# Kernel optimization log

Measured on AMD Instinct MI355X. Metric: run time of the kernel, lower is better.

Reference implementation:

```python
import jax, jax.numpy as jnp
import numpy as np
from jax import lax

H = 145; W = 145; BANDS = 200; D_MODEL = 128; NUM_CLASSES = 17
# Mamba2 defaults: expand=2, headdim=64, d_state=128, d_conv=4, ngroups=1
D_INNER = 256; NHEADS = 4; HEADDIM = 64; D_STATE = 128; D_CONV = 4
D_IN_PROJ = 2 * D_INNER + 2 * D_STATE + NHEADS  # 772
CONV_DIM = D_INNER + 2 * D_STATE                # 512


def _gelu(x):
    return jax.nn.gelu(x, approximate=False)


def _ln(x, g, b, eps=1e-5):
    m = jnp.mean(x, -1, keepdims=True)
    v = jnp.mean((x - m) ** 2, -1, keepdims=True)
    return (x - m) * lax.rsqrt(v + eps) * g + b


def _adaptive_pool_last(x, out):
    # PyTorch AdaptiveAvgPool semantics along the last axis via integral image
    L = x.shape[-1]
    i = np.arange(out)
    starts = (i * L) // out
    ends = -((-(i + 1) * L) // out)  # ceil((i+1)*L/out)
    cs = jnp.concatenate([jnp.zeros(x.shape[:-1] + (1,), x.dtype), jnp.cumsum(x, -1)], -1)
    return (cs[..., ends] - cs[..., starts]) / jnp.asarray(ends - starts, x.dtype)


def _mamba2(u, in_w, conv_w, conv_b, dt_bias, A_log, D, norm_w, out_w):
    # u: (L, D_MODEL). Faithful Mamba2 reference path (batch=1 squeezed).
    L = u.shape[0]
    zxbcdt = u @ in_w                      # (L, 772)
    z = zxbcdt[:, :D_INNER]                # (L, 256)
    xBC = zxbcdt[:, D_INNER:2 * D_INNER + 2 * D_STATE]  # (L, 512)
    dt = jax.nn.softplus(zxbcdt[:, -NHEADS:] + dt_bias)  # (L, 4)
    # causal depthwise conv1d, kernel D_CONV, then SiLU
    xp = jnp.pad(xBC, ((D_CONV - 1, 0), (0, 0)))
    xBC = sum(xp[k:k + L] * conv_w[:, k] for k in range(D_CONV)) + conv_b
    xBC = jax.nn.silu(xBC)
    xh = xBC[:, :D_INNER].reshape(L, NHEADS, HEADDIM)     # (L, h, p)
    Bm = xBC[:, D_INNER:D_INNER + D_STATE]                # (L, n)
    Cm = xBC[:, D_INNER + D_STATE:]                       # (L, n)
    A = -jnp.exp(A_log)                                   # (h,)

    def step(state, inp):
        dt_t, x_t, B_t, C_t = inp          # (h,), (h,p), (n,), (n,)
        dA = jnp.exp(dt_t * A)             # (h,)
        state = state * dA[:, None, None] + (dt_t[:, None] * x_t)[:, :, None] * B_t[None, None, :]
        y_t = jnp.einsum('hpn,n->hp', state, C_t)
        return state, y_t

    s0 = jnp.zeros((NHEADS, HEADDIM, D_STATE), u.dtype)
    _, y = lax.scan(step, s0, (dt, xh, Bm, Cm))           # y: (L, h, p)
    y = y + D[None, :, None] * xh
    y = y.reshape(L, D_INNER) * jax.nn.silu(z)            # gated
    y = y * lax.rsqrt(jnp.mean(y * y, -1, keepdims=True) + 1e-5) * norm_w  # RMSNormGated
    return y @ out_w                                      # (L, D_MODEL)


def _forward(x, ln_pre_g, ln_pre_b, fe_w1, fe_b1, fe_w2, fe_b2,
             cv_w1, cv_b1, cv_w2, cv_b2, mp_w, mp_b, mp_ln_g, mp_ln_b,
             m_in_w, m_conv_w, m_conv_b, m_dt_bias, m_A_log, m_D, m_norm_w, m_out_w,
             cls_ln_g, cls_ln_b, cls_w1, cls_b1, cls_w2, cls_b2, cls_w3, cls_b3):
    h, w, _ = x.shape
    xn = _ln(x, ln_pre_g, ln_pre_b)
    # MLP feature branch
    f = _gelu(xn @ fe_w1 + fe_b1)
    f = _gelu(f @ fe_w2 + fe_b2)                          # (h, w, 128)
    # conv branch
    c = jnp.transpose(xn, (2, 0, 1))[None]                # (1, bands, h, w)
    dn = ('NCHW', 'OIHW', 'NCHW')
    c = lax.conv_general_dilated(c, cv_w1, (1, 1), [(2, 2), (2, 2)], dimension_numbers=dn)
    c = _gelu(c + cv_b1[None, :, None, None])             # (1, 32, 147, 147)
    c = lax.conv_general_dilated(c, cv_w2, (1, 1), [(1, 1), (1, 1)], dimension_numbers=dn)
    c = _gelu(c + cv_b2[None, :, None, None])             # (1, 64, 147, 147)
    c = _adaptive_pool_last(c, W)                         # pool width -> 145
    c = _adaptive_pool_last(c.swapaxes(-1, -2), H).swapaxes(-1, -2)  # pool height
    conv_feat = jnp.transpose(c[0], (1, 2, 0))            # (145, 145, 64)
    comb = jnp.concatenate([f, conv_feat], -1).reshape(h * w, 192)
    p = _gelu(_ln(comb @ mp_w + mp_b, mp_ln_g, mp_ln_b))  # (L, d_model)
    m = _mamba2(p, m_in_w, m_conv_w, m_conv_b, m_dt_bias, m_A_log, m_D, m_norm_w, m_out_w)
    r = m.reshape(h, w, D_MODEL)
    o = _ln(r, cls_ln_g, cls_ln_b)
    o = _gelu(o @ cls_w1 + cls_b1)
    o = _gelu(o @ cls_w2 + cls_b2)
    return o @ cls_w3 + cls_b3                            # (h, w, num_classes)


def setup_inputs() -> dict:
    key = jax.random.key(0)
    ks = jax.random.split(key, 16)
    def n(k, shape, s=0.02):
        return jax.random.normal(k, shape, jnp.float32) * s
    return dict(
        x=jax.random.normal(ks[0], (H, W, BANDS), jnp.float32),
        ln_pre_g=jnp.ones((BANDS,), jnp.float32), ln_pre_b=jnp.zeros((BANDS,), jnp.float32),
        fe_w1=n(ks[1], (BANDS, 256)), fe_b1=jnp.zeros((256,), jnp.float32),
        fe_w2=n(ks[2], (256, 128)), fe_b2=jnp.zeros((128,), jnp.float32),
        cv_w1=n(ks[3], (32, BANDS, 3, 3)), cv_b1=jnp.zeros((32,), jnp.float32),
        cv_w2=n(ks[4], (64, 32, 3, 3)), cv_b2=jnp.zeros((64,), jnp.float32),
        mp_w=n(ks[5], (192, D_MODEL)), mp_b=jnp.zeros((D_MODEL,), jnp.float32),
        mp_ln_g=jnp.ones((D_MODEL,), jnp.float32), mp_ln_b=jnp.zeros((D_MODEL,), jnp.float32),
        m_in_w=n(ks[6], (D_MODEL, D_IN_PROJ)),
        m_conv_w=n(ks[7], (CONV_DIM, D_CONV), 0.2), m_conv_b=jnp.zeros((CONV_DIM,), jnp.float32),
        m_dt_bias=jnp.full((NHEADS,), -4.0, jnp.float32),
        m_A_log=jnp.log(jnp.linspace(1.0, 16.0, NHEADS)).astype(jnp.float32),
        m_D=jnp.ones((NHEADS,), jnp.float32),
        m_norm_w=jnp.ones((D_INNER,), jnp.float32),
        m_out_w=n(ks[8], (D_INNER, D_MODEL)),
        cls_ln_g=jnp.ones((D_MODEL,), jnp.float32), cls_ln_b=jnp.zeros((D_MODEL,), jnp.float32),
        cls_w1=n(ks[9], (D_MODEL, 128)), cls_b1=jnp.zeros((128,), jnp.float32),
        cls_w2=n(ks[10], (128, 64)), cls_b2=jnp.zeros((64,), jnp.float32),
        cls_w3=n(ks[11], (64, NUM_CLASSES)), cls_b3=jnp.zeros((NUM_CLASSES,), jnp.float32),
    )


def reference(x, ln_pre_g, ln_pre_b, fe_w1, fe_b1, fe_w2, fe_b2,
              cv_w1, cv_b1, cv_w2, cv_b2, mp_w, mp_b, mp_ln_g, mp_ln_b,
              m_in_w, m_conv_w, m_conv_b, m_dt_bias, m_A_log, m_D, m_norm_w, m_out_w,
              cls_ln_g, cls_ln_b, cls_w1, cls_b1, cls_w2, cls_b2, cls_w3, cls_b3):
    return _forward(x, ln_pre_g, ln_pre_b, fe_w1, fe_b1, fe_w2, fe_b2,
                    cv_w1, cv_b1, cv_w2, cv_b2, mp_w, mp_b, mp_ln_g, mp_ln_b,
                    m_in_w, m_conv_w, m_conv_b, m_dt_bias, m_A_log, m_D, m_norm_w, m_out_w,
                    cls_ln_g, cls_ln_b, cls_w1, cls_b1, cls_w2, cls_b2, cls_w3, cls_b3)
```

## Files before the change

### kernel.cpp

```cpp
#include <hip/hip_runtime.h>
#include <math.h>

#define HW 21025
#define Hdim 145
#define Wdim 145
#define NBANDS 200
#define CONVH 147
#define CONVHW 21609
#define QC 64
#define NCH 329
#define DTP 21056
#define SP 72
#define SSD_GRID 1344

typedef __attribute__((ext_vector_type(4))) float fv4;
typedef __attribute__((ext_vector_type(8))) short short8;

#define OFF_XN   ((size_t)0)
#define OFF_F1   ((size_t)4205000)
#define OFF_COMB ((size_t)9587400)
#define OFF_P    ((size_t)13624200)
#define OFF_ZX   ((size_t)16315400)
#define OFF_XBC  ((size_t)32546700)
#define OFF_S    ((size_t)43311500)
#define OFF_DT   ((size_t)54092172)
#define OFF_CT   ((size_t)54176396)
#define OFF_W    ((size_t)54177712)

__device__ __forceinline__ float gelu_f(float x){
    return 0.5f * x * (1.0f + erff(x * 0.70710678118654752440f));
}
__device__ __forceinline__ float silu_f(float x){
    return x / (1.0f + expf(-x));
}

__device__ __forceinline__ void bf16_split(float x, unsigned short& hs, unsigned short& ls){
    unsigned u = __float_as_uint(x);
    hs = (unsigned short)(u >> 16);
    float hif = __uint_as_float(u & 0xFFFF0000u);
    float lof = x - hif;
    ls = (unsigned short)(__float_as_uint(lof) >> 16);
}
__device__ __forceinline__ unsigned pack2(unsigned short a, unsigned short b){
    return (unsigned)a | ((unsigned)b << 16);
}
__device__ __forceinline__ unsigned packsplit(float x){
    unsigned short hs, ls;
    bf16_split(x, hs, ls);
    return ((unsigned)hs << 16) | (unsigned)ls;
}
__device__ __forceinline__ float unpackf(unsigned u){
    return __uint_as_float(u & 0xFFFF0000u) + __uint_as_float(u << 16);
}
__device__ __forceinline__ unsigned short bf16rnd(float x){
    unsigned u = __float_as_uint(x);
    unsigned r = u + 0x7FFFu + ((u >> 16) & 1u);
    return (unsigned short)(r >> 16);
}
__device__ __forceinline__ float bf16f(unsigned short h){
    return __uint_as_float((unsigned)h << 16);
}
__device__ __forceinline__ void unpack8(const unsigned* p, short8& h8, short8& l8){
    uint4 a = *reinterpret_cast<const uint4*>(p);
    uint4 b = *reinterpret_cast<const uint4*>(p + 4);
    unsigned v0 = a.x, v1 = a.y, v2 = a.z, v3 = a.w;
    unsigned v4 = b.x, v5 = b.y, v6 = b.z, v7 = b.w;
    h8[0]=(short)(v0>>16); l8[0]=(short)(v0&0xFFFFu);
    h8[1]=(short)(v1>>16); l8[1]=(short)(v1&0xFFFFu);
    h8[2]=(short)(v2>>16); l8[2]=(short)(v2&0xFFFFu);
    h8[3]=(short)(v3>>16); l8[3]=(short)(v3&0xFFFFu);
    h8[4]=(short)(v4>>16); l8[4]=(short)(v4&0xFFFFu);
    h8[5]=(short)(v5>>16); l8[5]=(short)(v5&0xFFFFu);
    h8[6]=(short)(v6>>16); l8[6]=(short)(v6&0xFFFFu);
    h8[7]=(short)(v7>>16); l8[7]=(short)(v7&0xFFFFu);
}

__device__ __forceinline__ bool gemm_decode(int bid, int NXB, int NYB, int& bx, int& by){
    int m = bid & 7;
    int r = bid >> 3;
    bx = r % NXB;
    by = (r / NXB) * 8 + m;
    return by < NYB;
}
__host__ __forceinline__ int gemm_grid(int NXB, int NYB){ return 8 * ((NYB + 7) / 8) * NXB; }

template<int ACT>
__global__ void ln_kernel(const float* __restrict__ in, const float* __restrict__ g,
                          const float* __restrict__ b, float* __restrict__ out, int D){
    int row = blockIdx.x, tid = threadIdx.x;
    const float* r = in + (size_t)row * D;
    float s = 0.f, s2 = 0.f;
    for (int i = tid; i < D; i += 256){ float v = r[i]; s += v; s2 += v*v; }
    __shared__ float r1[4], r2[4];
    #pragma unroll
    for (int o = 32; o > 0; o >>= 1){ s += __shfl_down(s, o); s2 += __shfl_down(s2, o); }
    if ((tid & 63) == 0){ r1[tid >> 6] = s; r2[tid >> 6] = s2; }
    __syncthreads();
    float S = r1[0] + r1[1] + r1[2] + r1[3];
    float S2 = r2[0] + r2[1] + r2[2] + r2[3];
    float mean = S / (float)D;
    float var = S2 / (float)D - mean * mean;
    float rs = rsqrtf(fmaxf(var, 0.f) + 1e-5f);
    float* o_ = out + (size_t)row * D;
    for (int i = tid; i < D; i += 256){
        float v = (r[i] - mean) * rs * g[i] + b[i];
        if (ACT == 1) v = gelu_f(v);
        o_[i] = v;
    }
}

template<int ACT, int MI, int ARMS>
__global__ __launch_bounds__(256) void gemm_mfma_w(const float* __restrict__ A, int lda,
                                                   const float* __restrict__ B, int ldb,
                                                   const float* __restrict__ bias,
                                                   const float* __restrict__ lng,
                                                   const float* __restrict__ lnb,
                                                   const float* __restrict__ arms_w,
                                                   float* __restrict__ C, int ldc,
                                                   int M, int N, int K, int NXB, int NYB){
    const int SA = 40;
    const int BM = MI * 32;
    __shared__ __align__(16) unsigned short Ah[BM * SA], Al[BM * SA];
    __shared__ __align__(16) unsigned short Bh[128 * SA], Bl[128 * SA];
    __shared__ float rs1[2][BM], rs2_[2][BM];
    __shared__ float ascale[BM];
    __shared__ float wn[256];
    int bx, by;
    if (!gemm_decode(blockIdx.x, NXB, NYB, bx, by)) return;
    int tid = threadIdx.x;
    int lane = tid & 63, wid = tid >> 6;
    int wy = wid >> 1, wx = wid & 1;
    int bm = by * BM, bn = bx * 128;
    int l15 = lane & 15, g = lane >> 4;

    if (ARMS){
        for (int i = tid; i < K && i < 256; i += 256) wn[i] = arms_w[i];
        int row = tid >> 2, seg = tid & 3;
        float ss = 0.f;
        if (row < BM && (bm + row) < M){
            const float* ar = A + (size_t)(bm + row) * lda + seg * (K >> 2);
            for (int k = 0; k < (K >> 2); k += 4){
                fv4 v = *reinterpret_cast<const fv4*>(ar + k);
                ss += v[0]*v[0] + v[1]*v[1] + v[2]*v[2] + v[3]*v[3];
            }
        }
        ss += __shfl_xor(ss, 1);
        ss += __shfl_xor(ss, 2);
        if ((tid & 3) == 0 && row < BM) ascale[row] = rsqrtf(ss / (float)K + 1e-5f);
        __syncthreads();
    }

    fv4 acc[MI][4];
    #pragma unroll
    for (int i = 0; i < MI; i++)
        #pragma unroll
        for (int j = 0; j < 4; j++) acc[i][j] = (fv4){0.f,0.f,0.f,0.f};

    int bcol = tid & 127;
    int bk16 = (tid >> 7) * 16;
    bool bcol_ok = (bn + bcol) < N;

    int nK = (K + 31) / 32;
    for (int ks = 0; ks < nK; ks++){
        int k0 = ks * 32;
        #pragma unroll
        for (int f = 0; f < MI; f++){
            int idx = tid * MI + f;
            int row = idx >> 3, qd = idx & 7;
            fv4 v = (fv4){0.f,0.f,0.f,0.f};
            if ((bm + row) < M && (k0 + qd * 4 + 4) <= K)
                v = *reinterpret_cast<const fv4*>(A + (size_t)(bm + row) * lda + k0 + qd * 4);
            if (ARMS) v *= ascale[row];
            unsigned short hs[4], ls[4];
            #pragma unroll
            for (int j = 0; j < 4; j++) bf16_split(v[j], hs[j], ls[j]);
            unsigned off = row * SA + qd * 4;
            *reinterpret_cast<uint2*>(&Ah[off]) = make_uint2(pack2(hs[0],hs[1]), pack2(hs[2],hs[3]));
            *reinterpret_cast<uint2*>(&Al[off]) = make_uint2(pack2(ls[0],ls[1]), pack2(ls[2],ls[3]));
        }
        {
            unsigned short hs[16], ls[16];
            #pragma unroll
            for (int j = 0; j < 16; j++){
                int kk = k0 + bk16 + j;
                float v = (bcol_ok && kk < K) ? B[(size_t)kk * ldb + bn + bcol] : 0.f;
                if (ARMS && kk < K) v *= wn[kk];
                bf16_split(v, hs[j], ls[j]);
            }
            unsigned off = bcol * SA + bk16;
            *reinterpret_cast<uint4*>(&Bh[off]) = make_uint4(pack2(hs[0],hs[1]), pack2(hs[2],hs[3]),
                                                             pack2(hs[4],hs[5]), pack2(hs[6],hs[7]));
            *reinterpret_cast<uint4*>(&Bh[off + 8]) = make_uint4(pack2(hs[8],hs[9]), pack2(hs[10],hs[11]),
                                                                 pack2(hs[12],hs[13]), pack2(hs[14],hs[15]));
            *reinterpret_cast<uint4*>(&Bl[off]) = make_uint4(pack2(ls[0],ls[1]), pack2(ls[2],ls[3]),
                                                             pack2(ls[4],ls[5]), pack2(ls[6],ls[7]));
            *reinterpret_cast<uint4*>(&Bl[off + 8]) = make_uint4(pack2(ls[8],ls[9]), pack2(ls[10],ls[11]),
                                                                 pack2(ls[12],ls[13]), pack2(ls[14],ls[15]));
        }
        __syncthreads();
        short8 afh[MI], afl[MI], bfh[4], bfl[4];
        #pragma unroll
        for (int mi = 0; mi < MI; mi++){
            unsigned off = (wy * (MI * 16) + mi * 16 + l15) * SA + g * 8;
            afh[mi] = *reinterpret_cast<const short8*>(&Ah[off]);
            afl[mi] = *reinterpret_cast<const short8*>(&Al[off]);
        }
        #pragma unroll
        for (int ni = 0; ni < 4; ni++){
            unsigned off = (wx * 64 + ni * 16 + l15) * SA + g * 8;
            bfh[ni] = *reinterpret_cast<const short8*>(&Bh[off]);
            bfl[ni] = *reinterpret_cast<const short8*>(&Bl[off]);
        }
        #pragma unroll
        for (int mi = 0; mi < MI; mi++)
            #pragma unroll
            for (int ni = 0; ni < 4; ni++){
                acc[mi][ni] = __builtin_amdgcn_mfma_f32_16x16x32_bf16(afh[mi], bfh[ni], acc[mi][ni], 0, 0, 0);
                acc[mi][ni] = __builtin_amdgcn_mfma_f32_16x16x32_bf16(afh[mi], bfl[ni], acc[mi][ni], 0, 0, 0);
                acc[mi][ni] = __builtin_amdgcn_mfma_f32_16x16x32_bf16(afl[mi], bfh[ni], acc[mi][ni], 0, 0, 0);
            }
        __syncthreads();
    }
    float bv[4], lgv[4], lbv[4];
    #pragma unroll
    for (int ni = 0; ni < 4; ni++){
        int cc = bn + wx * 64 + ni * 16 + l15;
        bool ok = cc < N;
        bv[ni]  = (bias && ok) ? bias[cc] : 0.f;
        if (ACT >= 2){ lgv[ni] = ok ? lng[cc] : 1.f; lbv[ni] = ok ? lnb[cc] : 0.f; }
    }
    if (ACT >= 2){
        #pragma unroll
        for (int mi = 0; mi < MI; mi++)
            #pragma unroll
            for (int j = 0; j < 4; j++){
                float s = 0.f, s2 = 0.f;
                #pragma unroll
                for (int ni = 0; ni < 4; ni++){
                    float v = acc[mi][ni][j] + bv[ni];
                    s += v; s2 += v * v;
                }
                #pragma unroll
                for (int o = 1; o < 16; o <<= 1){
                    s += __shfl_xor(s, o); s2 += __shfl_xor(s2, o);
                }
                int row = wy * (MI * 16) + mi * 16 + g * 4 + j;
                if (l15 == 0){ rs1[wx][row] = s; rs2_[wx][row] = s2; }
            }
        __syncthreads();
        #pragma unroll
        for (int mi = 0; mi < MI; mi++)
            #pragma unroll
            for (int j = 0; j < 4; j++){
                int row = wy * (MI * 16) + mi * 16 + g * 4 + j;
                int rr = bm + row;
                if (rr >= M) continue;
                float S = rs1[0][row] + rs1[1][row];
                float S2 = rs2_[0][row] + rs2_[1][row];
                float mean = S / 128.f;
                float var = S2 / 128.f - mean * mean;
                float rsq = rsqrtf(fmaxf(var, 0.f) + 1e-5f);
                #pragma unroll
                for (int ni = 0; ni < 4; ni++){
                    int cc = bn + wx * 64 + ni * 16 + l15;
                    float v = acc[mi][ni][j] + bv[ni];
                    v = (v - mean) * rsq * lgv[ni] + lbv[ni];
                    if (ACT == 3) v = gelu_f(v);
                    C[(size_t)rr * ldc + cc] = v;
                }
            }
    } else {
        #pragma unroll
        for (int mi = 0; mi < MI; mi++)
            #pragma unroll
            for (int ni = 0; ni < 4; ni++){
                int cc = bn + wx * 64 + ni * 16 + l15;
                if (cc >= N) continue;
                #pragma unroll
                for (int j = 0; j < 4; j++){
                    int rr = bm + wy * (MI * 16) + mi * 16 + g * 4 + j;
                    if (rr >= M) continue;
                    float v = acc[mi][ni][j] + bv[ni];
                    if (ACT == 1) v = gelu_f(v);
                    C[(size_t)rr * ldc + cc] = v;
                }
            }
    }
}

__global__ __launch_bounds__(256) void cls_tail(const float* __restrict__ A,
                                                const float* __restrict__ W2,
                                                const float* __restrict__ b2,
                                                const float* __restrict__ W3,
                                                const float* __restrict__ b3,
                                                float* __restrict__ out,
                                                int M, int NYB){
    const int SA = 40;
    __shared__ __align__(16) unsigned short Ah[64 * SA], Al[64 * SA];
    __shared__ __align__(16) unsigned short Bh[64 * SA], Bl[64 * SA];
    __shared__ __align__(16) unsigned short A2h[64 * 72], A2l[64 * 72];
    __shared__ __align__(16) unsigned short B3h[32 * 72], B3l[32 * 72];
    int bx, by;
    if (!gemm_decode(blockIdx.x, 1, NYB, bx, by)) return;
    int tid = threadIdx.x;
    int lane = tid & 63, wid = tid >> 6;
    int wy = wid >> 1, wx = wid & 1;
    int bm = by * 64;
    int l15 = lane & 15, g = lane >> 4;

    for (int e = tid; e < 2048; e += 256){
        int n = e >> 6, k = e & 63;
        float v = (n < 17) ? W3[(size_t)k * 17 + n] : 0.f;
        unsigned short hs, ls;
        bf16_split(v, hs, ls);
        B3h[n * 72 + k] = hs;
        B3l[n * 72 + k] = ls;
    }

    fv4 acc[2][2];
    #pragma unroll
    for (int mi = 0; mi < 2; mi++)
        #pragma unroll
        for (int ni = 0; ni < 2; ni++) acc[mi][ni] = (fv4){0.f,0.f,0.f,0.f};

    int bn_t = tid & 63;
    int bk8 = (tid >> 6) * 8;
    #pragma unroll
    for (int ks = 0; ks < 4; ks++){
        int k0 = ks * 32;
        #pragma unroll
        for (int f = 0; f < 2; f++){
            int idx = tid * 2 + f;
            int row = idx >> 3, qd = idx & 7;
            fv4 v = (fv4){0.f,0.f,0.f,0.f};
            if ((bm + row) < M)
                v = *reinterpret_cast<const fv4*>(A + (size_t)(bm + row) * 128 + k0 + qd * 4);
            unsigned short hs[4], ls[4];
            #pragma unroll
            for (int j = 0; j < 4; j++) bf16_split(v[j], hs[j], ls[j]);
            unsigned off = row * SA + qd * 4;
            *reinterpret_cast<uint2*>(&Ah[off]) = make_uint2(pack2(hs[0],hs[1]), pack2(hs[2],hs[3]));
            *reinterpret_cast<uint2*>(&Al[off]) = make_uint2(pack2(ls[0],ls[1]), pack2(ls[2],ls[3]));
        }
        {
            unsigned short hs[8], ls[8];
            #pragma unroll
            for (int j = 0; j < 8; j++){
                int kk = k0 + bk8 + j;
                float v = W2[(size_t)kk * 64 + bn_t];
                bf16_split(v, hs[j], ls[j]);
            }
            unsigned off = bn_t * SA + bk8;
            *reinterpret_cast<uint4*>(&Bh[off]) = make_uint4(pack2(hs[0],hs[1]), pack2(hs[2],hs[3]),
                                                             pack2(hs[4],hs[5]), pack2(hs[6],hs[7]));
            *reinterpret_cast<uint4*>(&Bl[off]) = make_uint4(pack2(ls[0],ls[1]), pack2(ls[2],ls[3]),
                                                             pack2(ls[4],ls[5]), pack2(ls[6],ls[7]));
        }
        __syncthreads();
        short8 afh[2], afl[2], bfh[2], bfl[2];
        #pragma unroll
        for (int mi = 0; mi < 2; mi++){
            unsigned off = (wy * 32 + mi * 16 + l15) * SA + g * 8;
            afh[mi] = *reinterpret_cast<const short8*>(&Ah[off]);
            afl[mi] = *reinterpret_cast<const short8*>(&Al[off]);
        }
        #pragma unroll
        for (int ni = 0; ni < 2; ni++){
            unsigned off = (wx * 32 + ni * 16 + l15) * SA + g * 8;
            bfh[ni] = *reinterpret_cast<const short8*>(&Bh[off]);
            bfl[ni] = *reinterpret_cast<const short8*>(&Bl[off]);
        }
        #pragma unroll
        for (int mi = 0; mi < 2; mi++)
            #pragma unroll
            for (int ni = 0; ni < 2; ni++){
                acc[mi][ni] = __builtin_amdgcn_mfma_f32_16x16x32_bf16(afh[mi], bfh[ni], acc[mi][ni], 0, 0, 0);
                acc[mi][ni] = __builtin_amdgcn_mfma_f32_16x16x32_bf16(afh[mi], bfl[ni], acc[mi][ni], 0, 0, 0);
                acc[mi][ni] = __builtin_amdgcn_mfma_f32_16x16x32_bf16(afl[mi], bfh[ni], acc[mi][ni], 0, 0, 0);
            }
        __syncthreads();
    }
    #pragma unroll
    for (int mi = 0; mi < 2; mi++)
        #pragma unroll
        for (int ni = 0; ni < 2; ni++){
            int col = wx * 32 + ni * 16 + l15;
            float bv = b2[col];
            #pragma unroll
            for (int j = 0; j < 4; j++){
                int row = wy * 32 + mi * 16 + g * 4 + j;
                float v = gelu_f(acc[mi][ni][j] + bv);
                unsigned short hs, ls;
                bf16_split(v, hs, ls);
                A2h[row * 72 + col] = hs;
                A2l[row * 72 + col] = ls;
            }
        }
    __syncthreads();
    fv4 acc3[2];
    acc3[0] = (fv4){0.f,0.f,0.f,0.f};
    acc3[1] = (fv4){0.f,0.f,0.f,0.f};
    #pragma unroll
    for (int ks = 0; ks < 2; ks++){
        unsigned aoff = (wid * 16 + l15) * 72 + ks * 32 + g * 8;
        short8 a2h = *reinterpret_cast<const short8*>(&A2h[aoff]);
        short8 a2l = *reinterpret_cast<const short8*>(&A2l[aoff]);
        #pragma unroll
        for (int ni = 0; ni < 2; ni++){
            unsigned boff = (ni * 16 + l15) * 72 + ks * 32 + g * 8;
            short8 b3h_ = *reinterpret_cast<const short8*>(&B3h[boff]);
            short8 b3l_ = *reinterpret_cast<const short8*>(&B3l[boff]);
            acc3[ni] = __builtin_amdgcn_mfma_f32_16x16x32_bf16(a2h, b3h_, acc3[ni], 0, 0, 0);
            acc3[ni] = __builtin_amdgcn_mfma_f32_16x16x32_bf16(a2h, b3l_, acc3[ni], 0, 0, 0);
            acc3[ni] = __builtin_amdgcn_mfma_f32_16x16x32_bf16(a2l, b3h_, acc3[ni], 0, 0, 0);
        }
    }
    #pragma unroll
    for (int ni = 0; ni < 2; ni++){
        int col = ni * 16 + l15;
        if (col >= 17) continue;
        float bv = b3[col];
        #pragma unroll
        for (int j = 0; j < 4; j++){
            int row = bm + wid * 16 + g * 4 + j;
            if (row >= M) continue;
            out[(size_t)row * 17 + col] = acc3[ni][j] + bv;
        }
    }
}

__global__ __launch_bounds__(256) void dt_from_p(const float* __restrict__ p,
                                                 const float* __restrict__ w,
                                                 const float* __restrict__ dtb,
                                                 float* __restrict__ dtbT){
    __shared__ float wl[512];
    int tid = threadIdx.x;
    for (int i = tid; i < 512; i += 256){
        int k = i >> 2, h = i & 3;
        wl[i] = w[(size_t)k * 772 + 768 + h];
// ... 268 lines not shown
__global__ __launch_bounds__(64) void ssd_phaseB(unsigned short* __restrict__ Sb,
                                                 const float* __restrict__ chunkT){
    __shared__ float e[NCH];
    int tid = threadIdx.x;
    int idx = blockIdx.x * 64 + tid;
    int h = idx >> 13, pn = idx & 8191;
    for (int c = tid; c < NCH; c += 64) e[c] = __expf(chunkT[c * 4 + h]);
    __syncthreads();
    #define ADDR_(cc) Sb[((size_t)((cc) * 4 + h)) * 8192 + pn]
    unsigned short r0 = ADDR_(0), r1 = ADDR_(1), r2 = ADDR_(2), r3 = ADDR_(3);
    float s = 0.f;
    int c = 0;
    for (; c + 8 <= NCH; c += 4){
        unsigned short n0 = ADDR_(c + 4), n1 = ADDR_(c + 5), n2 = ADDR_(c + 6), n3 = ADDR_(c + 7);
        ADDR_(c) = bf16rnd(s);     s = fmaf(s, e[c],     bf16f(r0));
        ADDR_(c + 1) = bf16rnd(s); s = fmaf(s, e[c + 1], bf16f(r1));
        ADDR_(c + 2) = bf16rnd(s); s = fmaf(s, e[c + 2], bf16f(r2));
        ADDR_(c + 3) = bf16rnd(s); s = fmaf(s, e[c + 3], bf16f(r3));
        r0 = n0; r1 = n1; r2 = n2; r3 = n3;
    }
    for (; c < NCH; c++){
        unsigned short nx = (c + 4 < NCH) ? ADDR_(c + 4) : (unsigned short)0;
        float loc = bf16f(r0); r0 = r1; r1 = r2; r2 = r3; r3 = nx;
        ADDR_(c) = bf16rnd(s);
        s = fmaf(s, e[c], loc);
    }
    #undef ADDR_
}

__global__ __launch_bounds__(256) void ssd_phaseC(const unsigned* __restrict__ xbcp,
                                                  const float* __restrict__ zx,
                                                  const float* __restrict__ dtbT,
                                                  const float* __restrict__ A_log,
                                                  const float* __restrict__ Dvec,
                                                  const unsigned short* __restrict__ Sb,
                                                  float* __restrict__ y){
    __shared__ __align__(16) unsigned short U0[64 * SP];
    __shared__ __align__(16) unsigned short U1h[64 * SP], U1l[64 * SP];
    __shared__ float cum[64], dth[64];
    int c, h;
    if (!ssd_decode(blockIdx.x, c, h)) return;
    int t0 = c * QC, Q = min(QC, HW - t0);
    int tid = threadIdx.x;
    chunk_cumsum_t(dtbT, t0, Q, h, A_log, cum, dth);
    int lane = tid & 63, wid = tid >> 6;
    int wy = wid >> 1, wx = wid & 1;
    int l15 = lane & 15, g = lane >> 4;

    int trow[2], srow[2], prow[2];
    #pragma unroll
    for (int i = 0; i < 2; i++){
        trow[i] = min(t0 + wy * 32 + i * 16 + l15, HW - 1);
        srow[i] = min(t0 + wx * 32 + i * 16 + l15, HW - 1);
        prow[i] = wx * 32 + i * 16 + l15;
    }

    fv4 accG[2][2], accA[2][2];
    #pragma unroll
    for (int mi = 0; mi < 2; mi++)
        #pragma unroll
        for (int ni = 0; ni < 2; ni++){ accG[mi][ni] = (fv4){0.f,0.f,0.f,0.f}; accA[mi][ni] = (fv4){0.f,0.f,0.f,0.f}; }

    const unsigned short* Sbase = Sb + (size_t)(c * 4 + h) * 8192;
    #pragma unroll
    for (int k0 = 0; k0 < 128; k0 += 32){
        short8 ah[2], al[2], bh[2], bl[2], sh[2];
        #pragma unroll
        for (int mi = 0; mi < 2; mi++)
            unpack8(xbcp + (size_t)trow[mi] * 512 + 384 + k0 + g * 8, ah[mi], al[mi]);
        #pragma unroll
        for (int ni = 0; ni < 2; ni++){
            unpack8(xbcp + (size_t)srow[ni] * 512 + 256 + k0 + g * 8, bh[ni], bl[ni]);
            sh[ni] = *reinterpret_cast<const short8*>(Sbase + prow[ni] * 128 + k0 + g * 8);
        }
        #pragma unroll
        for (int mi = 0; mi < 2; mi++)
            #pragma unroll
            for (int ni = 0; ni < 2; ni++){
                accG[mi][ni] = __builtin_amdgcn_mfma_f32_16x16x32_bf16(ah[mi], bh[ni], accG[mi][ni], 0, 0, 0);
                accG[mi][ni] = __builtin_amdgcn_mfma_f32_16x16x32_bf16(ah[mi], bl[ni], accG[mi][ni], 0, 0, 0);
                accG[mi][ni] = __builtin_amdgcn_mfma_f32_16x16x32_bf16(al[mi], bh[ni], accG[mi][ni], 0, 0, 0);
                accA[mi][ni] = __builtin_amdgcn_mfma_f32_16x16x32_bf16(ah[mi], sh[ni], accA[mi][ni], 0, 0, 0);
                accA[mi][ni] = __builtin_amdgcn_mfma_f32_16x16x32_bf16(al[mi], sh[ni], accA[mi][ni], 0, 0, 0);
            }
    }
    #pragma unroll
    for (int mi = 0; mi < 2; mi++)
        #pragma unroll
        for (int ni = 0; ni < 2; ni++)
            #pragma unroll
            for (int j = 0; j < 4; j++){
                int t = wy * 32 + mi * 16 + g * 4 + j;
                int s = wx * 32 + ni * 16 + l15;
                float pv = 0.f;
                if (s <= t && s < Q)
                    pv = accG[mi][ni][j] * __expf(cum[t] - cum[s]) * dth[s];
                U0[t * SP + s] = bf16rnd(pv);
            }
    for (int e2 = tid; e2 < 2048; e2 += 256){
        int pp = e2 & 63, sp = e2 >> 6;
        int s0 = 2 * sp;
        unsigned v0 = (s0 < Q)     ? xbcp[(size_t)(t0 + s0) * 512 + h * 64 + pp] : 0u;
        unsigned v1 = (s0 + 1 < Q) ? xbcp[(size_t)(t0 + s0 + 1) * 512 + h * 64 + pp] : 0u;
        *reinterpret_cast<unsigned*>(&U1h[pp * SP + s0]) = pack2((unsigned short)(v0 >> 16), (unsigned short)(v1 >> 16));
        *reinterpret_cast<unsigned*>(&U1l[pp * SP + s0]) = pack2((unsigned short)(v0 & 0xFFFFu), (unsigned short)(v1 & 0xFFFFu));
    }
    __syncthreads();
    fv4 accY[2][2];
    #pragma unroll
    for (int mi = 0; mi < 2; mi++)
        #pragma unroll
        for (int ni = 0; ni < 2; ni++)
            #pragma unroll
            for (int j = 0; j < 4; j++){
                int t = wy * 32 + mi * 16 + g * 4 + j;
                accY[mi][ni][j] = __expf(cum[t]) * accA[mi][ni][j];
            }
    #pragma unroll
    for (int kk = 0; kk < 2; kk++){
        short8 ph[2], xh[2], xl[2];
        #pragma unroll
        for (int mi = 0; mi < 2; mi++){
            unsigned off = (wy * 32 + mi * 16 + l15) * SP + kk * 32 + g * 8;
            ph[mi] = *reinterpret_cast<const short8*>(&U0[off]);
        }
        #pragma unroll
        for (int ni = 0; ni < 2; ni++){
            unsigned off = (wx * 32 + ni * 16 + l15) * SP + kk * 32 + g * 8;
            xh[ni] = *reinterpret_cast<const short8*>(&U1h[off]);
            xl[ni] = *reinterpret_cast<const short8*>(&U1l[off]);
        }
        #pragma unroll
        for (int mi = 0; mi < 2; mi++)
            #pragma unroll
            for (int ni = 0; ni < 2; ni++){
                accY[mi][ni] = __builtin_amdgcn_mfma_f32_16x16x32_bf16(ph[mi], xh[ni], accY[mi][ni], 0, 0, 0);
                accY[mi][ni] = __builtin_amdgcn_mfma_f32_16x16x32_bf16(ph[mi], xl[ni], accY[mi][ni], 0, 0, 0);
            }
    }
    float Dh = Dvec[h];
    #pragma unroll
    for (int mi = 0; mi < 2; mi++)
        #pragma unroll
        for (int ni = 0; ni < 2; ni++)
            #pragma unroll
            for (int j = 0; j < 4; j++){
                int t = wy * 32 + mi * 16 + g * 4 + j;
                if (t >= Q) continue;
                int p = wx * 32 + ni * 16 + l15;
                float xv = unpackf(xbcp[(size_t)(t0 + t) * 512 + h * 64 + p]);
                float zv = zx[(size_t)(t0 + t) * 772 + h * 64 + p];
                y[(size_t)(t0 + t) * 256 + h * 64 + p] = (accY[mi][ni][j] + Dh * xv) * silu_f(zv);
            }
}

extern "C" void kernel_launch(void* const* d_in, const int* in_sizes, int n_in,
                              void* d_out, int out_size, void* d_ws, size_t ws_size,
                              hipStream_t stream){
    (void)in_sizes; (void)n_in; (void)out_size; (void)ws_size;
    const float* x        = (const float*)d_in[0];
    const float* ln_pre_g = (const float*)d_in[1];
    const float* ln_pre_b = (const float*)d_in[2];
    const float* fe_w1    = (const float*)d_in[3];
    const float* fe_b1    = (const float*)d_in[4];
    const float* fe_w2    = (const float*)d_in[5];
    const float* fe_b2    = (const float*)d_in[6];
    const float* cv_w1    = (const float*)d_in[7];
    const float* cv_b1    = (const float*)d_in[8];
    const float* cv_w2    = (const float*)d_in[9];
    const float* cv_b2    = (const float*)d_in[10];
    const float* mp_w     = (const float*)d_in[11];
    const float* mp_b     = (const float*)d_in[12];
    const float* mp_ln_g  = (const float*)d_in[13];
    const float* mp_ln_b  = (const float*)d_in[14];
    const float* m_in_w   = (const float*)d_in[15];
    const float* m_conv_w = (const float*)d_in[16];
    const float* m_conv_b = (const float*)d_in[17];
    const float* m_dtb    = (const float*)d_in[18];
    const float* m_A_log  = (const float*)d_in[19];
    const float* m_D      = (const float*)d_in[20];
    const float* m_norm_w = (const float*)d_in[21];
    const float* m_out_w  = (const float*)d_in[22];
    const float* cls_ln_g = (const float*)d_in[23];
    const float* cls_ln_b = (const float*)d_in[24];
    const float* cls_w1   = (const float*)d_in[25];
    const float* cls_b1   = (const float*)d_in[26];
    const float* cls_w2   = (const float*)d_in[27];
    const float* cls_b2   = (const float*)d_in[28];
    const float* cls_w3   = (const float*)d_in[29];
    const float* cls_b3   = (const float*)d_in[30];

    float* ws   = (float*)d_ws;
    float* xn   = ws + OFF_XN;
    float* f1   = ws + OFF_F1;
    float* comb = ws + OFF_COMB;
    float* p    = ws + OFF_P;
    float* zx   = ws + OFF_ZX;
    unsigned* xbcp = (unsigned*)(ws + OFF_XBC);
    unsigned short* Sb = (unsigned short*)(ws + OFF_S);
    float* dtbT = ws + OFF_DT;
    float* chkT = ws + OFF_CT;
    float* c1h  = ws + OFF_XBC;
    float* c2h  = ws + OFF_XBC + 691488;
    float* ybuf = ws + OFF_F1;
    float* cls0 = ws + OFF_XN;
    float* cls1 = ws + OFF_P;
    unsigned short* W1h = (unsigned short*)(ws + OFF_W);
    unsigned short* W1l = (unsigned short*)(ws + OFF_W + 32256);
    unsigned short* W2h = (unsigned short*)(ws + OFF_W + 64512);
    unsigned short* W2l = (unsigned short*)(ws + OFF_W + 73728);
    const float* NUL = (const float*)nullptr;

    prep_w<200, 32, 7><<<(32 * 2016 + 255) / 256, 256, 0, stream>>>(cv_w1, W1h, W1l);
    prep_w<32, 64, 1><<<(64 * 288 + 255) / 256, 256, 0, stream>>>(cv_w2, W2h, W2l);
    ln_kernel<0><<<HW, 256, 0, stream>>>(x, ln_pre_g, ln_pre_b, xn, NBANDS);
    gemm_mfma_w<1, 4, 0><<<gemm_grid(2, 165), 256, 0, stream>>>(xn, 200, fe_w1, 256, fe_b1,
        NUL, NUL, NUL, f1, 256, HW, 256, 200, 2, 165);
    gemm_mfma_w<1, 2, 0><<<gemm_grid(1, 329), 256, 0, stream>>>(f1, 256, fe_w2, 128, fe_b2,
        NUL, NUL, NUL, comb, 192, HW, 128, 256, 1, 329);
    conv_mfma<200, 32, 2, 7, 1><<<dim3(3, CONVH), 256, 0, stream>>>(xn, Hdim, Wdim, W1h, W1l, cv_b1, c1h);
    conv_mfma<32, 64, 1, 1, 2><<<dim3(3, CONVH), 256, 0, stream>>>(c1h, CONVH, CONVH, W2h, W2l, cv_b2, c2h);
    pool_kernel<<<(HW * 64 + 255) / 256, 256, 0, stream>>>(c2h, comb);
    gemm_mfma_w<3, 2, 0><<<gemm_grid(1, 329), 256, 0, stream>>>(comb, 192, mp_w, 128, mp_b,
        mp_ln_g, mp_ln_b, NUL, p, 128, HW, 128, 192, 1, 329);
    gemm_mfma_w<0, 4, 0><<<gemm_grid(6, 165), 256, 0, stream>>>(p, 128, m_in_w, 772,
        NUL, NUL, NUL, NUL, zx, 772, HW, 768, 128, 6, 165);
    dt_from_p<<<(HW + 63) / 64, 256, 0, stream>>>(p, m_in_w, m_dtb, dtbT);
    conv1d_tiled<<<dim3(4, NCH), 256, 0, stream>>>(zx, m_conv_w, m_conv_b, xbcp);
    ssd_phaseA<<<SSD_GRID, 256, 0, stream>>>(xbcp, dtbT, m_A_log, Sb, chkT);
    ssd_phaseB<<<512, 64, 0, stream>>>(Sb, chkT);
    ssd_phaseC<<<SSD_GRID, 256, 0, stream>>>(xbcp, zx, dtbT, m_A_log, m_D, Sb, ybuf);
    gemm_mfma_w<2, 2, 1><<<gemm_grid(1, 329), 256, 0, stream>>>(ybuf, 256, m_out_w, 128,
        NUL, cls_ln_g, cls_ln_b, m_norm_w, cls0, 128, HW, 128, 256, 1, 329);
    gemm_mfma_w<1, 2, 0><<<gemm_grid(1, 329), 256, 0, stream>>>(cls0, 128, cls_w1, 128, cls_b1,
        NUL, NUL, NUL, cls1, 128, HW, 128, 128, 1, 329);
    cls_tail<<<gemm_grid(1, 329), 256, 0, stream>>>(cls1, cls_w2, cls_b2, cls_w3, cls_b3,
        (float*)d_out, HW, 329);
}
```

Baseline: 475.0 us.

## Replace LDS-staged GEMM with direct-load MFMA GEMM using pre-split packed weights

```diff
diff --git a/kernel.cpp b/kernel.cpp
--- a/kernel.cpp
+++ b/kernel.cpp
@@ -26,6 +26,15 @@
 #define OFF_DT   ((size_t)54092172)
 #define OFF_CT   ((size_t)54176396)
 #define OFF_W    ((size_t)54177712)
+#define OFF_WG   ((size_t)54260656)
+
+#define WG_FE1   0
+#define WG_FE2   57344
+#define WG_MP    90112
+#define WG_IN    114688
+#define WG_OUT   212992
+#define WG_CLS1  245760
+#define WG_TOTAL 262144
 
 __device__ __forceinline__ float gelu_f(float x){
     return 0.5f * x * (1.0f + erff(x * 0.70710678118654752440f));
@@ -74,6 +83,14 @@
     h8[6]=(short)(v6>>16); l8[6]=(short)(v6&0xFFFFu);
     h8[7]=(short)(v7>>16); l8[7]=(short)(v7&0xFFFFu);
 }
+__device__ __forceinline__ void split8f(fv4 a0, fv4 a1, short8& h8, short8& l8){
+    unsigned short hs, ls;
+    #pragma unroll
+    for (int j = 0; j < 4; j++){
+        bf16_split(a0[j], hs, ls); h8[j] = (short)hs; l8[j] = (short)ls;
+        bf16_split(a1[j], hs, ls); h8[4 + j] = (short)hs; l8[4 + j] = (short)ls;
+    }
+}
 
 __device__ __forceinline__ bool gemm_decode(int bid, int NXB, int NYB, int& bx, int& by){
     int m = bid & 7;
@@ -109,182 +126,126 @@
     }
 }
 
-template<int ACT, int MI, int ARMS>
-__global__ __launch_bounds__(256) void gemm_mfma_w(const float* __restrict__ A, int lda,
-                                                   const float* __restrict__ B, int ldb,
+__global__ void prep_fc(const float* __restrict__ fe_w1, const float* __restrict__ fe_w2,
+                        const float* __restrict__ mp_w, const float* __restrict__ in_w,
+                        const float* __restrict__ out_w, const float* __restrict__ cls_w1,
+                        unsigned* __restrict__ Wg){
+    int idx = blockIdx.x * 256 + threadIdx.x;
+    if (idx >= WG_TOTAL) return;
+    const float* src; int Ksrc, Kp, ld, local;
+    if (idx < WG_FE2)      { src = fe_w1;  Ksrc = 200; Kp = 224; ld = 256; local = idx; }
+    else if (idx < WG_MP)  { src = fe_w2;  Ksrc = 256; Kp = 256; ld = 128; local = idx - WG_FE2; }
+    else if (idx < WG_IN)  { src = mp_w;   Ksrc = 192; Kp = 192; ld = 128; local = idx - WG_MP; }
+    else if (idx < WG_OUT) { src = in_w;   Ksrc = 128; Kp = 128; ld = 772; local = idx - WG_IN; }
+    else if (idx < WG_CLS1){ src = out_w;  Ksrc = 256; Kp = 256; ld = 128; local = idx - WG_OUT; }
+    else                   { src = cls_w1; Ksrc = 128; Kp = 128; ld = 128; local = idx - WG_CLS1; }
+    int col = local / Kp, k = local % Kp;
+    float v = (k < Ksrc) ? src[(size_t)k * ld + col] : 0.f;
+    Wg[idx] = packsplit(v);
+}
+
+template<int ACT, int MF>
+__global__ __launch_bounds__(256) void gemm_direct(const float* __restrict__ A, int lda,
+                                                   const unsigned* __restrict__ Wg,
                                                    const float* __restrict__ bias,
                                                    const float* __restrict__ lng,
                                                    const float* __restrict__ lnb,
-                                                   const float* __restrict__ arms_w,
                                                    float* __restrict__ C, int ldc,
-                                                   int M, int N, int K, int NXB, int NYB){
-    const int SA = 40;
-    const int BM = MI * 32;
-    __shared__ __align__(16) unsigned short Ah[BM * SA], Al[BM * SA];
-    __shared__ __align__(16) unsigned short Bh[128 * SA], Bl[128 * SA];
-    __shared__ float rs1[2][BM], rs2_[2][BM];
-    __shared__ float ascale[BM];
-    __shared__ float wn[256];
+                                                   int M, int N, int K, int Kp,
+                                                   int NXB, int NYB){
     int bx, by;
     if (!gemm_decode(blockIdx.x, NXB, NYB, bx, by)) return;
     int tid = threadIdx.x;
-    int lane = tid & 63, wid = tid >> 6;
-    int wy = wid >> 1, wx = wid & 1;
-    int bm = by * BM, bn = bx * 128;
+    int w = tid >> 6, lane = tid & 63;
     int l15 = lane & 15, g = lane >> 4;
-
-    if (ARMS){
-        for (int i = tid; i < K && i < 256; i += 256) wn[i] = arms_w[i];
-        int row = tid >> 2, seg = tid & 3;
-        float ss = 0.f;
-        if (row < BM && (bm + row) < M){
-            const float* ar = A + (size_t)(bm + row) * lda + seg * (K >> 2);
-            for (int k = 0; k < (K >> 2); k += 4){
-                fv4 v = *reinterpret_cast<const fv4*>(ar + k);
-                ss += v[0]*v[0] + v[1]*v[1] + v[2]*v[2] + v[3]*v[3];
-            }
-        }
-        ss += __shfl_xor(ss, 1);
-        ss += __shfl_xor(ss, 2);
-        if ((tid & 3) == 0 && row < BM) ascale[row] = rsqrtf(ss / (float)K + 1e-5f);
-        __syncthreads();
-    }
-
-    fv4 acc[MI][4];
-    #pragma unroll
-    for (int i = 0; i < MI; i++)
-        #pragma unroll
-        for (int j = 0; j < 4; j++) acc[i][j] = (fv4){0.f,0.f,0.f,0.f};
-
-    int bcol = tid & 127;
-    int bk16 = (tid >> 7) * 16;
-    bool bcol_ok = (bn + bcol) < N;
-
-    int nK = (K + 31) / 32;
-    for (int ks = 0; ks < nK; ks++){
-        int k0 = ks * 32;
-        #pragma unroll
-        for (int f = 0; f < MI; f++){
-            int idx = tid * MI + f;
-            int row = idx >> 3, qd = idx & 7;
-            fv4 v = (fv4){0.f,0.f,0.f,0.f};
-            if ((bm + row) < M && (k0 + qd * 4 + 4) <= K)
-                v = *reinterpret_cast<const fv4*>(A + (size_t)(bm + row) * lda + k0 + qd * 4);
-            if (ARMS) v *= ascale[row];
-            unsigned short hs[4], ls[4];
-            #pragma unroll
-            for (int j = 0; j < 4; j++) bf16_split(v[j], hs[j], ls[j]);
-            unsigned off = row * SA + qd * 4;
-            *reinterpret_cast<uint2*>(&Ah[off]) = make_uint2(pack2(hs[0],hs[1]), pack2(hs[2],hs[3]));
-            *reinterpret_cast<uint2*>(&Al[off]) = make_uint2(pack2(ls[0],ls[1]), pack2(ls[2],ls[3]));
-        }
-        {
-            unsigned short hs[16], ls[16];
-            #pragma unroll
-            for (int j = 0; j < 16; j++){
-                int kk = k0 + bk16 + j;
-                float v = (bcol_ok && kk < K) ? B[(size_t)kk * ldb + bn + bcol] : 0.f;
-                if (ARMS && kk < K) v *= wn[kk];
-                bf16_split(v, hs[j], ls[j]);
-            }
-            unsigned off = bcol * SA + bk16;
-            *reinterpret_cast<uint4*>(&Bh[off]) = make_uint4(pack2(hs[0],hs[1]), pack2(hs[2],hs[3]),
-                                                             pack2(hs[4],hs[5]), pack2(hs[6],hs[7]));
-            *reinterpret_cast<uint4*>(&Bh[off + 8]) = make_uint4(pack2(hs[8],hs[9]), pack2(hs[10],hs[11]),
-                                                                 pack2(hs[12],hs[13]), pack2(hs[14],hs[15]));
-            *reinterpret_cast<uint4*>(&Bl[off]) = make_uint4(pack2(ls[0],ls[1]), pack2(ls[2],ls[3]),
-                                                             pack2(ls[4],ls[5]), pack2(ls[6],ls[7]));
-            *reinterpret_cast<uint4*>(&Bl[off + 8]) = make_uint4(pack2(ls[8],ls[9]), pack2(ls[10],ls[11]),
-                                                                 pack2(ls[12],ls[13]), pack2(ls[14],ls[15]));
-        }
-        __syncthreads();
-        short8 afh[MI], afl[MI], bfh[4], bfl[4];
-        #pragma unroll
-        for (int mi = 0; mi < MI; mi++){
-            unsigned off = (wy * (MI * 16) + mi * 16 + l15) * SA + g * 8;
-            afh[mi] = *reinterpret_cast<const short8*>(&Ah[off]);
-            afl[mi] = *reinterpret_cast<const short8*>(&Al[off]);
-        }
-        #pragma unroll
-        for (int ni = 0; ni < 4; ni++){
-            unsigned off = (wx * 64 + ni * 16 + l15) * SA + g * 8;
-            bfh[ni] = *reinterpret_cast<const short8*>(&Bh[off]);
-            bfl[ni] = *reinterpret_cast<const short8*>(&Bl[off]);
-        }
-        #pragma unroll
-        for (int mi = 0; mi < MI; mi++)
-            #pragma unroll
-            for (int ni = 0; ni < 4; ni++){
-                acc[mi][ni] = __builtin_amdgcn_mfma_f32_16x16x32_bf16(afh[mi], bfh[ni], acc[mi][ni], 0, 0, 0);
-                acc[mi][ni] = __builtin_amdgcn_mfma_f32_16x16x32_bf16(afh[mi], bfl[ni], acc[mi][ni], 0, 0, 0);
-                acc[mi][ni] = __builtin_amdgcn_mfma_f32_16x16x32_bf16(afl[mi], bfh[ni], acc[mi][ni], 0, 0, 0);
-            }
-        __syncthreads();
-    }
-    float bv[4], lgv[4], lbv[4];
-    #pragma unroll
-    for (int ni = 0; ni < 4; ni++){
-        int cc = bn + wx * 64 + ni * 16 + l15;
-        bool ok = cc < N;
-        bv[ni]  = (bias && ok) ? bias[cc] : 0.f;
-        if (ACT >= 2){ lgv[ni] = ok ? lng[cc] : 1.f; lbv[ni] = ok ? lnb[cc] : 0.f; }
-    }
-    if (ACT >= 2){
-        #pragma unroll
-        for (int mi = 0; mi < MI; mi++)
+    int bn = bx * 128;
+    int bm_w = by * (4 * MF * 16) + w * (MF * 16);
+
+    int arow[MF];
+    #pragma unroll
+    for (int mf = 0; mf < MF; mf++) arow[mf] = min(bm_w + mf * 16 + l15, M - 1);
+
+    fv4 acc[MF][8];
+    #pragma unroll
+    for (int mf = 0; mf < MF; mf++)
+        #pragma unroll
+        for (int ni = 0; ni < 8; ni++) acc[mf][ni] = (fv4){0.f,0.f,0.f,0.f};
+
+    for (int k0 = 0; k0 < K; k0 += 32){
+        short8 ah[MF], al[MF];
+        #pragma unroll
+        for (int mf = 0; mf < MF; mf++){
+            const float* ap = A + (size_t)arow[mf] * lda + k0 + g * 8;
+            fv4 a0 = (fv4){0.f,0.f,0.f,0.f}, a1 = (fv4){0.f,0.f,0.f,0.f};
+            if (k0 + g * 8 + 4 <= K) a0 = *reinterpret_cast<const fv4*>(ap);
+            if (k0 + g * 8 + 8 <= K) a1 = *reinterpret_cast<const fv4*>(ap + 4);
+            split8f(a0, a1, ah[mf], al[mf]);
+        }
+        #pragma unroll
+        for (int ni = 0; ni < 8; ni++){
+            const unsigned* bp = Wg + (size_t)(bn + ni * 16 + l15) * Kp + k0 + g * 8;
+            short8 bh, bl;
+            unpack8(bp, bh, bl);
+            #pragma unroll
+            for (int mf = 0; mf < MF; mf++){
+                acc[mf][ni] = __builtin_amdgcn_mfma_f32_16x16x32_bf16(ah[mf], bh, acc[mf][ni], 0, 0, 0);
+                acc[mf][ni] = __builtin_amdgcn_mfma_f32_16x16x32_bf16(ah[mf], bl, acc[mf][ni], 0, 0, 0);
+                acc[mf][ni] = __builtin_amdgcn_mfma_f32_16x16x32_bf16(al[mf], bh, acc[mf][ni], 0, 0, 0);
+            }
+        }
+    }
+    float bv[8], lgv[8], lbv[8];
+    #pragma unroll
+    for (int ni = 0; ni < 8; ni++){
+        int cc = bn + ni * 16 + l15;
+        bv[ni] = bias ? bias[cc] : 0.f;
+        if (ACT >= 2){ lgv[ni] = lng[cc]; lbv[ni] = lnb[cc]; }
+    }
+    #pragma unroll
+    for (int mf = 0; mf < MF; mf++){
+        if (ACT >= 2){
             #pragma unroll
             for (int j = 0; j < 4; j++){
+                int row = bm_w + mf * 16 + g * 4 + j;
                 float s = 0.f, s2 = 0.f;
                 #pragma unroll
-                for (int ni = 0; ni < 4; ni++){
-                    float v = acc[mi][ni][j] + bv[ni];
+                for (int ni = 0; ni < 8; ni++){
+                    float v = acc[mf][ni][j] + bv[ni];
                     s += v; s2 += v * v;
                 }
                 #pragma unroll
                 for (int o = 1; o < 16; o <<= 1){
                     s += __shfl_xor(s, o); s2 += __shfl_xor(s2, o);
                 }
-                int row = wy * (MI * 16) + mi * 16 + g * 4 + j;
-                if (l15 == 0){ rs1[wx][row] = s; rs2_[wx][row] = s2; }
-            }
-        __syncthreads();
-        #pragma unroll
-        for (int mi = 0; mi < MI; mi++)
-            #pragma unroll
-            for (int j = 0; j < 4; j++){
-                int row = wy * (MI * 16) + mi * 16 + g * 4 + j;
-                int rr = bm + row;
-                if (rr >= M) continue;
-                float S = rs1[0][row] + rs1[1][row];
-                float S2 = rs2_[0][row] + rs2_[1][row];
-                float mean = S / 128.f;
-                float var = S2 / 128.f - mean * mean;
+                float mean = s / 128.f;
+                float var = s2 / 128.f - mean * mean;
                 float rsq = rsqrtf(fmaxf(var, 0.f) + 1e-5f);
-                #pragma unroll
-                for (int ni = 0; ni < 4; ni++){
-                    int cc = bn + wx * 64 + ni * 16 + l15;
-                    float v = acc[mi][ni][j] + bv[ni];
-                    v = (v - mean) * rsq * lgv[ni] + lbv[ni];
-                    if (ACT == 3) v = gelu_f(v);
-                    C[(size_t)rr * ldc + cc] = v;
+                if (row < M){
+                    #pragma unroll
+                    for (int ni = 0; ni < 8; ni++){
+                        int cc = bn + ni * 16 + l15;
+                        float v = acc[mf][ni][j] + bv[ni];
+                        v = (v - mean) * rsq * lgv[ni] + lbv[ni];
+                        if (ACT == 3) v = gelu_f(v);
+                        C[(size_t)row * ldc + cc] = v;
+                    }
                 }
             }
-    } else {
-        #pragma unroll
-        for (int mi = 0; mi < MI; mi++)
-            #pragma unroll
-            for (int ni = 0; ni < 4; ni++){
-                int cc = bn + wx * 64 + ni * 16 + l15;
+        } else {
+            #pragma unroll
+            for (int ni = 0; ni < 8; ni++){
+                int cc = bn + ni * 16 + l15;
                 if (cc >= N) continue;
                 #pragma unroll
                 for (int j = 0; j < 4; j++){
-                    int rr = bm + wy * (MI * 16) + mi * 16 + g * 4 + j;
-                    if (rr >= M) continue;
-                    float v = acc[mi][ni][j] + bv[ni];
+                    int row = bm_w + mf * 16 + g * 4 + j;
+                    if (row >= M) continue;
+                    float v = acc[mf][ni][j] + bv[ni];
                     if (ACT == 1) v = gelu_f(v);
-                    C[(size_t)rr * ldc + cc] = v;
+                    C[(size_t)row * ldc + cc] = v;
                 }
             }
+        }
     }
 }
 
@@ -859,6 +820,20 @@
                 float zv = zx[(size_t)(t0 + t) * 772 + h * 64 + p];
                 y[(size_t)(t0 + t) * 256 + h * 64 + p] = (accY[mi][ni][j] + Dh * xv) * silu_f(zv);
             }
+}
+
+__global__ void rms_kernel(float* __restrict__ y, const float* __restrict__ nw){
+    int row = blockIdx.x, tid = threadIdx.x;
+    float v = y[(size_t)row * 256 + tid];
+    float s = v * v;
+    __shared__ float r1[4];
+    #pragma unroll
+    for (int o = 32; o > 0; o >>= 1) s += __shfl_down(s, o);
+    if ((tid & 63) == 0) r1[tid >> 6] = s;
+    __syncthreads();
+    float S = r1[0] + r1[1] + r1[2] + r1[3];
+    float rs = rsqrtf(S / 256.f + 1e-5f);
+    y[(size_t)row * 256 + tid] = v * rs * nw[tid];
 }
 
 extern "C" void kernel_launch(void* const* d_in, const int* in_sizes, int n_in,
@@ -916,31 +891,34 @@
     unsigned short* W1l = (unsigned short*)(ws + OFF_W + 32256);
     unsigned short* W2h = (unsigned short*)(ws + OFF_W + 64512);
     unsigned short* W2l = (unsigned short*)(ws + OFF_W + 73728);
+    unsigned* Wg = (unsigned*)(ws + OFF_WG);
     const float* NUL = (const float*)nullptr;
 
     prep_w<200, 32, 7><<<(32 * 2016 + 255) / 256, 256, 0, stream>>>(cv_w1, W1h, W1l);
     prep_w<32, 64, 1><<<(64 * 288 + 255) / 256, 256, 0, stream>>>(cv_w2, W2h, W2l);
+    prep_fc<<<WG_TOTAL / 256, 256, 0, stream>>>(fe_w1, fe_w2, mp_w, m_in_w, m_out_w, cls_w1, Wg);
     ln_kernel<0><<<HW, 256, 0, stream>>>(x, ln_pre_g, ln_pre_b, xn, NBANDS);
-    gemm_mfma_w<1, 4, 0><<<gemm_grid(2, 165), 256, 0, stream>>>(xn, 200, fe_w1, 256, fe_b1,
-        NUL, NUL, NUL, f1, 256, HW, 256, 200, 2, 165);
-    gemm_mfma_w<1, 2, 0><<<gemm_grid(1, 329), 256, 0, stream>>>(f1, 256, fe_w2, 128, fe_b2,
-        NUL, NUL, NUL, comb, 192, HW, 128, 256, 1, 329);
+    gemm_direct<1, 2><<<gemm_grid(2, 165), 256, 0, stream>>>(xn, 200, Wg + WG_FE1, fe_b1,
+        NUL, NUL, f1, 256, HW, 256, 200, 224, 2, 165);
+    gemm_direct<1, 1><<<gemm_grid(1, 329), 256, 0, stream>>>(f1, 256, Wg + WG_FE2, fe_b2,
+        NUL, NUL, comb, 192, HW, 128, 256, 256, 1, 329);
     conv_mfma<200, 32, 2, 7, 1><<<dim3(3, CONVH), 256, 0, stream>>>(xn, Hdim, Wdim, W1h, W1l, cv_b1, c1h);
     conv_mfma<32, 64, 1, 1, 2><<<dim3(3, CONVH), 256, 0, stream>>>(c1h, CONVH, CONVH, W2h, W2l, cv_b2, c2h);
     pool_kernel<<<(HW * 64 + 255) / 256, 256, 0, stream>>>(c2h, comb);
-    gemm_mfma_w<3, 2, 0><<<gemm_grid(1, 329), 256, 0, stream>>>(comb, 192, mp_w, 128, mp_b,
-        mp_ln_g, mp_ln_b, NUL, p, 128, HW, 128, 192, 1, 329);
-    gemm_mfma_w<0, 4, 0><<<gemm_grid(6, 165), 256, 0, stream>>>(p, 128, m_in_w, 772,
-        NUL, NUL, NUL, NUL, zx, 772, HW, 768, 128, 6, 165);
+    gemm_direct<3, 1><<<gemm_grid(1, 329), 256, 0, stream>>>(comb, 192, Wg + WG_MP, mp_b,
+        mp_ln_g, mp_ln_b, p, 128, HW, 128, 192, 192, 1, 329);
+    gemm_direct<0, 2><<<gemm_grid(6, 165), 256, 0, stream>>>(p, 128, Wg + WG_IN, NUL,
+        NUL, NUL, zx, 772, HW, 768, 128, 128, 6, 165);
     dt_from_p<<<(HW + 63) / 64, 256, 0, stream>>>(p, m_in_w, m_dtb, dtbT);
     conv1d_tiled<<<dim3(4, NCH), 256, 0, stream>>>(zx, m_conv_w, m_conv_b, xbcp);
     ssd_phaseA<<<SSD_GRID, 256, 0, stream>>>(xbcp, dtbT, m_A_log, Sb, chkT);
     ssd_phaseB<<<512, 64, 0, stream>>>(Sb, chkT);
     ssd_phaseC<<<SSD_GRID, 256, 0, stream>>>(xbcp, zx, dtbT, m_A_log, m_D, Sb, ybuf);
-    gemm_mfma_w<2, 2, 1><<<gemm_grid(1, 329), 256, 0, stream>>>(ybuf, 256, m_out_w, 128,
-        NUL, cls_ln_g, cls_ln_b, m_norm_w, cls0, 128, HW, 128, 256, 1, 329);
-    gemm_mfma_w<1, 2, 0><<<gemm_grid(1, 329), 256, 0, stream>>>(cls0, 128, cls_w1, 128, cls_b1,
-        NUL, NUL, NUL, cls1, 128, HW, 128, 128, 1, 329);
+    rms_kernel<<<HW, 256, 0, stream>>>(ybuf, m_norm_w);
+    gemm_direct<2, 1><<<gemm_grid(1, 329), 256, 0, stream>>>(ybuf, 256, Wg + WG_OUT, NUL,
+        cls_ln_g, cls_ln_b, cls0, 128, HW, 128, 256, 256, 1, 329);
+    gemm_direct<1, 1><<<gemm_grid(1, 329), 256, 0, stream>>>(cls0, 128, Wg + WG_CLS1, cls_b1,
+        NUL, NUL, cls1, 128, HW, 128, 128, 128, 1, 329);
     cls_tail<<<gemm_grid(1, 329), 256, 0, stream>>>(cls1, cls_w2, cls_b2, cls_w3, cls_b3,
         (float*)d_out, HW, 329);
 }
```

Result: slower. 534.1 us (+12.4%).
